# Kernel optimization log

Hardware: AMD Instinct MI355X
Metric: run time of the kernel (lower is better)

The kernel has to match this reference:

```python
import jax, jax.numpy as jnp
import numpy as np

N, E = 50000, 640000
DIN, DH, DOUT = 128, 256, 128


def _glorot(k, i, o):
    return jax.random.normal(k, (i, o), jnp.float32) / np.sqrt(i)


def setup_inputs() -> dict:
    key = jax.random.key(0)
    ks = jax.random.split(key, 12)
    return {
        "x": jax.random.normal(ks[0], (N, DIN), jnp.float32),
        "edge_index": jax.random.randint(ks[1], (2, E), 0, N, dtype=jnp.int32),
        # SAGEConv 1: in -> hidden (lin_l on aggregated w/ bias, lin_r on root)
        "W1l": _glorot(ks[2], DIN, DH), "b1l": jnp.zeros((DH,), jnp.float32), "W1r": _glorot(ks[3], DIN, DH),
        "g1": jnp.ones((DH,), jnp.float32), "be1": jnp.zeros((DH,), jnp.float32),
        # skip projection (in != hidden)
        "Wsk": _glorot(ks[4], DIN, DH), "bsk": jnp.zeros((DH,), jnp.float32),
        # SAGEConv 2: hidden -> hidden
        "W2l": _glorot(ks[5], DH, DH), "b2l": jnp.zeros((DH,), jnp.float32), "W2r": _glorot(ks[6], DH, DH),
        "g2": jnp.ones((DH,), jnp.float32), "be2": jnp.zeros((DH,), jnp.float32),
        # SAGEConv 3: hidden -> out
        "W3l": _glorot(ks[7], DH, DOUT), "b3l": jnp.zeros((DOUT,), jnp.float32), "W3r": _glorot(ks[8], DH, DOUT),
    }


def _sage_conv(x, src, dst, Wl, bl, Wr, n):
    # mean aggregation of source features into destination nodes
    msg = x[src]                                                 # [E, d]
    agg = jax.ops.segment_sum(msg, dst, num_segments=n)          # [N, d]
    cnt = jax.ops.segment_sum(jnp.ones((src.shape[0],), x.dtype), dst, num_segments=n)
    agg = agg / jnp.maximum(cnt, 1.0)[:, None]
    return agg @ Wl + bl + x @ Wr


def _layernorm(x, g, b):
    mu = jnp.mean(x, axis=-1, keepdims=True)
    var = jnp.mean((x - mu) ** 2, axis=-1, keepdims=True)
    return (x - mu) * jax.lax.rsqrt(var + 1e-5) * g + b


def reference(x, edge_index, W1l, b1l, W1r, g1, be1, Wsk, bsk,
              W2l, b2l, W2r, g2, be2, W3l, b3l, W3r):
    src, dst = edge_index[0], edge_index[1]
    n = x.shape[0]
    # layer 0: conv -> LN -> relu -> (dropout p=0, eval) -> skip via projection
    h = _sage_conv(x, src, dst, W1l, b1l, W1r, n)
    h = jax.nn.relu(_layernorm(h, g1, be1))
    h = h + (x @ Wsk + bsk)
    # layer 1: conv -> LN -> relu -> residual add (shapes match)
    h2 = _sage_conv(h, src, dst, W2l, b2l, W2r, n)
    h2 = jax.nn.relu(_layernorm(h2, g2, be2)) + h
    # final conv (no norm/act)
    return _sage_conv(h2, src, dst, W3l, b3l, W3r, n)
```

## Files before the change

### kernel.cpp

```cpp
#include <hip/hip_runtime.h>


typedef float floatx4 __attribute__((ext_vector_type(4)));
typedef float floatx2 __attribute__((ext_vector_type(2)));
typedef short bf16x8 __attribute__((ext_vector_type(8)));

__device__ inline unsigned short f2bf(float f) {
    unsigned u = __float_as_uint(f);
    unsigned r = (u + 0x7fffu + ((u >> 16) & 1u)) >> 16;
    return (unsigned short)r;
}
__device__ inline float bf2f_lo(unsigned v) { return __uint_as_float(v << 16); }
__device__ inline float bf2f_hi(unsigned v) { return __uint_as_float(v & 0xffff0000u); }

__device__ inline void gl_lds16(const void* g, void* l) {
    __builtin_amdgcn_global_load_lds((const __attribute__((address_space(1))) unsigned int*)g,
                                     (__attribute__((address_space(3))) unsigned int*)l,
                                     16, 0, 0);
}

__global__ void hist_kernel(const int* __restrict__ dst, int* __restrict__ cnt, int E) {
    int i = blockIdx.x * blockDim.x + threadIdx.x;
    if (i < E) atomicAdd(&cnt[dst[i]], 1);
}

#define SCAN_CHUNK 2048

__global__ __launch_bounds__(256) void scan_blocksums(const int* __restrict__ cnt,
                                                      int* __restrict__ bsum, int N) {
    __shared__ int sh[256];
    int t = threadIdx.x;
    int base = blockIdx.x * SCAN_CHUNK + t * 8;
    int s = 0;
#pragma unroll
    for (int i = 0; i < 8; i++) {
        int idx = base + i;
        if (idx < N) s += cnt[idx];
    }
    sh[t] = s;
    __syncthreads();
    for (int off = 1; off < 256; off <<= 1) {
        int v = (t >= off) ? sh[t - off] : 0;
        __syncthreads();
        sh[t] += v;
        __syncthreads();
    }
    if (t == 255) bsum[blockIdx.x] = sh[255];
}

__global__ __launch_bounds__(256) void scan_bsums(const int* __restrict__ bsum,
                                                  int* __restrict__ boff, int NB,
                                                  int* __restrict__ rowptr, int N, int E) {
    __shared__ int sh[256];
    int t = threadIdx.x;
    int v = (t < NB) ? bsum[t] : 0;
    sh[t] = v;
    __syncthreads();
    for (int off = 1; off < 256; off <<= 1) {
        int u = (t >= off) ? sh[t - off] : 0;
        __syncthreads();
        sh[t] += u;
        __syncthreads();
    }
    if (t < NB) boff[t] = sh[t] - v;
    if (t == 0) rowptr[N] = E;
}

__global__ __launch_bounds__(256) void scan_final(const int* __restrict__ cnt,
                                                  const int* __restrict__ boff,
                                                  int* __restrict__ rowptr,
                                                  int* __restrict__ cursor,
                                                  float* __restrict__ invdeg, int N) {
    __shared__ int sh[256];
    int t = threadIdx.x;
    int base = blockIdx.x * SCAN_CHUNK + t * 8;
    int c[8];
    int s = 0;
#pragma unroll
    for (int i = 0; i < 8; i++) {
        int idx = base + i;
        c[i] = (idx < N) ? cnt[idx] : 0;
        s += c[i];
    }
    sh[t] = s;
    __syncthreads();
    for (int off = 1; off < 256; off <<= 1) {
        int v = (t >= off) ? sh[t - off] : 0;
        __syncthreads();
        sh[t] += v;
        __syncthreads();
    }
    int run = boff[blockIdx.x] + sh[t] - s;
#pragma unroll
    for (int i = 0; i < 8; i++) {
        int idx = base + i;
        if (idx < N) {
            rowptr[idx] = run;
            cursor[idx] = run;
            invdeg[idx] = 1.0f / (float)(c[i] > 1 ? c[i] : 1);
            run += c[i];
        }
    }
}

__global__ void scatter_kernel(const int* __restrict__ src, const int* __restrict__ dst,
                               int* __restrict__ cursor, int* __restrict__ col, int E) {
    int i = blockIdx.x * blockDim.x + threadIdx.x;
    if (i < E) {
        int p = atomicAdd(&cursor[dst[i]], 1);
        col[p] = src[i];
    }
}

__global__ void prep_weights(const float* __restrict__ W1l, const float* __restrict__ W1r,
                             const float* __restrict__ Wsk, const float* __restrict__ W2l,
                             const float* __restrict__ W2r, const float* __restrict__ W3l,
                             const float* __restrict__ W3r, const float* __restrict__ b1l,
                             const float* __restrict__ bsk,
                             unsigned short* __restrict__ WtC, unsigned short* __restrict__ Wt2,
                             unsigned short* __restrict__ Wt3, float* __restrict__ biasC) {
    int i = blockIdx.x * blockDim.x + threadIdx.x;
    if (i < 32768) {
        int k = i >> 8, n = i & 255;
        WtC[n * 256 + k] = f2bf(W1l[i]);
    } else if (i < 65536) {
        int j = i - 32768, k = j >> 8, n = j & 255;
        WtC[n * 256 + 128 + k] = f2bf(W1r[j]);
    } else if (i < 98304) {
        int j = i - 65536, k = j >> 8, n = j & 255;
        WtC[(256 + n) * 256 + 128 + k] = f2bf(Wsk[j]);
    } else if (i < 131072) {
        int j = i - 98304, k = j >> 8, n = j & 255;
        WtC[(256 + n) * 256 + k] = 0;
    } else if (i < 196608) {
        int j = i - 131072, k = j >> 8, n = j & 255;
        Wt2[n * 512 + k] = f2bf(W2l[j]);
    } else if (i < 262144) {
        int j = i - 196608, k = j >> 8, n = j & 255;
        Wt2[n * 512 + 256 + k] = f2bf(W2r[j]);
    } else if (i < 294912) {
        int j = i - 262144, k = j >> 7, n = j & 127;
        Wt3[n * 256 + k] = f2bf(W3l[j]);
    } else if (i < 327680) {
        int j = i - 294912, k = j >> 7, n = j & 127;
        Wt3[(128 + n) * 256 + k] = f2bf(W3r[j]);
    } else if (i < 328192) {
        int j = i - 327680;
        biasC[j] = (j < 256) ? b1l[j] : bsk[j - 256];
    }
}

__global__ void cvt_x2(const float* __restrict__ x, unsigned short* __restrict__ A1cat,
                       unsigned char* __restrict__ X8, int total32) {
    int i = blockIdx.x * blockDim.x + threadIdx.x;
    if (i >= total32) return;
    int r = i >> 5, c4 = (i & 31) * 4;
    float4 v = *(const float4*)(x + (size_t)r * 128 + c4);
    ushort4 o;
    o.x = f2bf(v.x); o.y = f2bf(v.y); o.z = f2bf(v.z); o.w = f2bf(v.w);
    *(ushort4*)(A1cat + (size_t)r * 256 + 128 + c4) = o;
    unsigned wpk = 0;
    wpk = __builtin_amdgcn_cvt_pk_fp8_f32(v.x, v.y, wpk, false);
    wpk = __builtin_amdgcn_cvt_pk_fp8_f32(v.z, v.w, wpk, true);
    *(unsigned*)(X8 + (size_t)r * 128 + c4) = wpk;
}

__device__ inline void accum_fp8(uint2 v, float m, float* a) {
    floatx2 p;
    p = __builtin_amdgcn_cvt_pk_f32_fp8(v.x, false); a[0] = fmaf(m, p.x, a[0]); a[1] = fmaf(m, p.y, a[1]);
    p = __builtin_amdgcn_cvt_pk_f32_fp8(v.x, true);  a[2] = fmaf(m, p.x, a[2]); a[3] = fmaf(m, p.y, a[3]);
    p = __builtin_amdgcn_cvt_pk_f32_fp8(v.y, false); a[4] = fmaf(m, p.x, a[4]); a[5] = fmaf(m, p.y, a[5]);
    p = __builtin_amdgcn_cvt_pk_f32_fp8(v.y, true);  a[6] = fmaf(m, p.x, a[6]); a[7] = fmaf(m, p.y, a[7]);
}

template <int RSB>
__global__ __launch_bounds__(256) void agg_fp8_c(const int* __restrict__ rowptr,
                                                 const int* __restrict__ col,
                                                 const float* __restrict__ invdeg,
                                                 const unsigned char* __restrict__ T8,
                                                 unsigned short* __restrict__ out, int ostride, int N) {
    int wid = (blockIdx.x * blockDim.x + threadIdx.x) >> 6;
    int lane = threadIdx.x & 63;
    if (wid >= N) return;
    int co = blockIdx.y * 64;
    int sub = lane & 7;
    int g = lane >> 3;
    const unsigned char* To = T8 + co + sub * 8;
    int s = rowptr[wid], e = rowptr[wid + 1];
    float a[8] = {0.f, 0.f, 0.f, 0.f, 0.f, 0.f, 0.f, 0.f};
    for (int j = s + g; j < e; j += 32) {
        int j1 = (j + 8 < e) ? j + 8 : j;
        int j2 = (j + 16 < e) ? j + 16 : j;
        int j3 = (j + 24 < e) ? j + 24 : j;
        float m1 = (j + 8 < e) ? 1.f : 0.f;
        float m2 = (j + 16 < e) ? 1.f : 0.f;
        float m3 = (j + 24 < e) ? 1.f : 0.f;
        int c0 = col[j], c1 = col[j1], c2 = col[j2], c3 = col[j3];
        uint2 v0 = *(const uint2*)(To + (size_t)c0 * RSB);
        uint2 v1 = *(const uint2*)(To + (size_t)c1 * RSB);
        uint2 v2 = *(const uint2*)(To + (size_t)c2 * RSB);
        uint2 v3 = *(const uint2*)(To + (size_t)c3 * RSB);
        accum_fp8(v0, 1.f, a);
        accum_fp8(v1, m1, a);
        accum_fp8(v2, m2, a);
        accum_fp8(v3, m3, a);
    }
#pragma unroll
    for (int i = 0; i < 8; i++) {
        a[i] += __shfl_xor(a[i], 8, 64);
        a[i] += __shfl_xor(a[i], 16, 64);
        a[i] += __shfl_xor(a[i], 32, 64);
    }
    if (g == 0) {
        float inv = invdeg[wid];
        uint4 o;
        o.x = (unsigned)f2bf(a[0] * inv) | ((unsigned)f2bf(a[1] * inv) << 16);
        o.y = (unsigned)f2bf(a[2] * inv) | ((unsigned)f2bf(a[3] * inv) << 16);
        o.z = (unsigned)f2bf(a[4] * inv) | ((unsigned)f2bf(a[5] * inv) << 16);
        o.w = (unsigned)f2bf(a[6] * inv) | ((unsigned)f2bf(a[7] * inv) << 16);
        *(uint4*)(out + (size_t)wid * ostride + co + sub * 8) = o;
    }
}

__global__ __launch_bounds__(256) void agg_fin_c(const int* __restrict__ rowptr,
                                                 const int* __restrict__ col,
                                                 const float* __restrict__ invdeg,
                                                 const unsigned short* __restrict__ T,
                                                 const float* __restrict__ R,
                                                 float* __restrict__ out, int N) {
    int wid = (blockIdx.x * blockDim.x + threadIdx.x) >> 6;
    int lane = threadIdx.x & 63;
    if (wid >= N) return;
    int co2 = blockIdx.y * 32;
    int sub = lane & 7;
    int g = lane >> 3;
    const unsigned short* To = T + co2 + sub * 4;
    int s = rowptr[wid], e = rowptr[wid + 1];
    float a0 = 0.f, a1 = 0.f, a2 = 0.f, a3 = 0.f;
    for (int j = s + g; j < e; j += 32) {
        int j1 = (j + 8 < e) ? j + 8 : j;
        int j2 = (j + 16 < e) ? j + 16 : j;
        int j3 = (j + 24 < e) ? j + 24 : j;
        float m1 = (j + 8 < e) ? 1.f : 0.f;
        float m2 = (j + 16 < e) ? 1.f : 0.f;
        float m3 = (j + 24 < e) ? 1.f : 0.f;
        int c0 = col[j], c1 = col[j1], c2 = col[j2], c3 = col[j3];
        uint2 v0 = *(const uint2*)(To + (size_t)c0 * 128);
        uint2 v1 = *(const uint2*)(To + (size_t)c1 * 128);
        uint2 v2 = *(const uint2*)(To + (size_t)c2 * 128);
        uint2 v3 = *(const uint2*)(To + (size_t)c3 * 128);
        a0 += bf2f_lo(v0.x); a1 += bf2f_hi(v0.x); a2 += bf2f_lo(v0.y); a3 += bf2f_hi(v0.y);
        a0 = fmaf(m1, bf2f_lo(v1.x), a0); a1 = fmaf(m1, bf2f_hi(v1.x), a1);
        a2 = fmaf(m1, bf2f_lo(v1.y), a2); a3 = fmaf(m1, bf2f_hi(v1.y), a3);
        a0 = fmaf(m2, bf2f_lo(v2.x), a0); a1 = fmaf(m2, bf2f_hi(v2.x), a1);
        a2 = fmaf(m2, bf2f_lo(v2.y), a2); a3 = fmaf(m2, bf2f_hi(v2.y), a3);
        a0 = fmaf(m3, bf2f_lo(v3.x), a0); a1 = fmaf(m3, bf2f_hi(v3.x), a1);
        a2 = fmaf(m3, bf2f_lo(v3.y), a2); a3 = fmaf(m3, bf2f_hi(v3.y), a3);
    }
#pragma unroll
    for (int off = 8; off < 64; off <<= 1) {
        a0 += __shfl_xor(a0, off, 64);
        a1 += __shfl_xor(a1, off, 64);
        a2 += __shfl_xor(a2, off, 64);
        a3 += __shfl_xor(a3, off, 64);
    }
    if (g == 0) {
        float inv = invdeg[wid];
        float4 r = *(const float4*)(R + (size_t)wid * 128 + co2 + sub * 4);
        float4 o;
        o.x = a0 * inv + r.x;
        o.y = a1 * inv + r.y;
        o.z = a2 * inv + r.z;
        o.w = a3 * inv + r.w;
        *(float4*)(out + (size_t)wid * 128 + co2 + sub * 4) = o;
    }
}

template <int KIT, int NPAN, int MODE>
__global__ __launch_bounds__(512) void gemm_fused(
    const unsigned short* __restrict__ A, int lda,
    const unsigned short* __restrict__ B, int ldb,
    const float* __restrict__ bias,
    const float* __restrict__ gamma, const float* __restrict__ beta,
    const unsigned short* __restrict__ resid,
    unsigned short* __restrict__ outb,
    unsigned char* __restrict__ h8,
    float* __restrict__ outf, int M) {
    constexpr int COLS = NPAN * 256;
    constexpr int LNW = COLS + 8;
    constexpr int STAGE_E = 128 * 64;
    constexpr int STAGE_F = 2 * STAGE_E / 2;
    constexpr int SMEM_F = (STAGE_F > 32 * LNW) ? STAGE_F : 32 * LNW;
    __shared__ __align__(16) float smemf[SMEM_F];
    unsigned short* sbase = (unsigned short*)smemf;

    int t = threadIdx.x;
    int lane = t & 63, w = t >> 6;
    int bm = blockIdx.x * 128;
    int wm = (w & 1) * 64, wn = (w >> 1) * 64;
    int m16 = lane & 15, kq = lane >> 4;

    floatx4 acc[NPAN][4][4];
#pragma unroll
    for (int p = 0; p < NPAN; p++)
#pragma unroll
        for (int i = 0; i < 4; i++)
#pragma unroll
            for (int j = 0; j < 4; j++) acc[p][i][j] = (floatx4){0.f, 0.f, 0.f, 0.f};

    const int s_row0 = t >> 3;
    const int s_j = t & 7;

    auto stage = [&](int kt, int bsel) {
        unsigned short* s = sbase + bsel * STAGE_E;
        int k0 = kt * 64;
#pragma unroll
        for (int i = 0; i < 2; i++) {
            int row = s_row0 + i * 64;
            int kc = s_j ^ (row & 7);
            int rowA = bm + row;
            if (rowA > M - 1) rowA = M - 1;
            gl_lds16(A + (size_t)rowA * lda + k0 + kc * 8, (void*)&s[(size_t)(i * 512 + t) * 8]);
        }
    };

    stage(0, 0);
    __syncthreads();
    for (int kt = 0; kt < KIT; kt++) {
        if (kt + 1 < KIT) stage(kt + 1, (kt & 1) ^ 1);
        const unsigned short* sA = sbase + (kt & 1) * STAGE_E;
#pragma unroll
        for (int ks = 0; ks < 2; ks++) {
            int kcl = (ks << 2) | kq;
            bf16x8 af[4];
#pragma unroll
            for (int mi = 0; mi < 4; mi++)
                af[mi] = *(const bf16x8*)&sA[(wm + mi * 16 + m16) * 64 + (kcl ^ (m16 & 7)) * 8];
#pragma unroll
            for (int p = 0; p < NPAN; p++) {
                if (MODE == 0 && p == 1 && kt * 64 < 128) continue;
                const unsigned short* Bp = B + (size_t)(wn + p * 256) * ldb + kt * 64;
                bf16x8 bf[4];
#pragma unroll
                for (int ni = 0; ni < 4; ni++)
                    bf[ni] = *(const bf16x8*)&Bp[(size_t)(ni * 16 + m16) * ldb + kcl * 8];
#pragma unroll
                for (int mi = 0; mi < 4; mi++)
#pragma unroll
                    for (int ni = 0; ni < 4; ni++)
                        acc[p][mi][ni] =
                            __builtin_amdgcn_mfma_f32_16x16x32_bf16(af[mi], bf[ni], acc[p][mi][ni], 0, 0, 0);
            }
        }
        __syncthreads();
    }

    float* lnb = smemf;
    int c4 = lane * 4;
    float4 bu = {0.f, 0.f, 0.f, 0.f}, bs = {0.f, 0.f, 0.f, 0.f};
    float4 gv = {0.f, 0.f, 0.f, 0.f}, bv = {0.f, 0.f, 0.f, 0.f};
    float4 b3 = {0.f, 0.f, 0.f, 0.f};
    if (MODE == 0) {
        bu = *(const float4*)&bias[c4];
        bs = *(const float4*)&bias[256 + c4];
        gv = *(const float4*)&gamma[c4];
        bv = *(const float4*)&beta[c4];
    } else if (MODE == 1) {
        bu = *(const float4*)&bias[c4];
        gv = *(const float4*)&gamma[c4];
        bv = *(const float4*)&beta[c4];
    } else {
        if (lane >= 32) b3 = *(const float4*)&bias[c4 - 128];
    }

#pragma unroll
    for (int g4 = 0; g4 < 4; g4++) {
        if (wm == (g4 >> 1) * 64) {
            int mi0 = (g4 & 1) * 2;
#pragma unroll
            for (int p = 0; p < NPAN; p++)
#pragma unroll
                for (int mm = 0; mm < 2; mm++)
#pragma unroll
                    for (int ni = 0; ni < 4; ni++)
#pragma unroll
                        for (int r = 0; r < 4; r++)
                            lnb[(mm * 16 + kq * 4 + r) * LNW + wn + p * 256 + ni * 16 + m16] =
                                acc[p][mi0 + mm][ni][r];
        }
        __syncthreads();
#pragma unroll
        for (int rr = 0; rr < 4; rr++) {
            int lrow = w * 4 + rr;
            int grow = bm + g4 * 32 + lrow;
            bool valid = grow < M;
            float4 u = *(const float4*)&lnb[lrow * LNW + c4];
            if (MODE <= 1) {
                u.x += bu.x; u.y += bu.y; u.z += bu.z; u.w += bu.w;
                float s1 = (u.x + u.y) + (u.z + u.w);
                float s2 = (u.x * u.x + u.y * u.y) + (u.z * u.z + u.w * u.w);
#pragma unroll
                for (int off = 1; off < 64; off <<= 1) {
                    s1 += __shfl_xor(s1, off, 64);
                    s2 += __shfl_xor(s2, off, 64);
                }
                float mu = s1 * (1.f / 256.f);
                float var = s2 * (1.f / 256.f) - mu * mu;
                float rs = rsqrtf(var + 1e-5f);
                float a0, a1, a2, a3;
                if (MODE == 0) {
                    float4 sv = *(const float4*)&lnb[lrow * LNW + 256 + c4];
                    a0 = sv.x + bs.x; a1 = sv.y + bs.y; a2 = sv.z + bs.z; a3 = sv.w + bs.w;
                } else {
                    int gr = valid ? grow : M - 1;
                    uint2 hv = *(const uint2*)(resid + (size_t)gr * 512 + c4);
                    a0 = bf2f_lo(hv.x); a1 = bf2f_hi(hv.x); a2 = bf2f_lo(hv.y); a3 = bf2f_hi(hv.y);
                }
                float o0 = fmaxf((u.x - mu) * rs * gv.x + bv.x, 0.f) + a0;
                float o1 = fmaxf((u.y - mu) * rs * gv.y + bv.y, 0.f) + a1;
                float o2 = fmaxf((u.z - mu) * rs * gv.z + bv.z, 0.f) + a2;
                float o3 = fmaxf((u.w - mu) * rs * gv.w + bv.w, 0.f) + a3;
                if (valid) {
                    ushort4 o;
                    o.x = f2bf(o0); o.y = f2bf(o1); o.z = f2bf(o2); o.w = f2bf(o3);
                    *(ushort4*)(outb + (size_t)grow * 512 + c4) = o;
                    if (MODE == 0) {
                        unsigned wpk = 0;
                        wpk = __builtin_amdgcn_cvt_pk_fp8_f32(o0, o1, wpk, false);
                        wpk = __builtin_amdgcn_cvt_pk_fp8_f32(o2, o3, wpk, true);
                        *(unsigned*)(h8 + (size_t)grow * 256 + c4) = wpk;
                    }
                }
            } else {
                if (valid) {
                    if (lane < 32) {
                        ushort4 o;
                        o.x = f2bf(u.x); o.y = f2bf(u.y); o.z = f2bf(u.z); o.w = f2bf(u.w);
                        *(ushort4*)(outb + (size_t)grow * 128 + c4) = o;
                    } else {
                        float4 o;
                        o.x = u.x + b3.x; o.y = u.y + b3.y; o.z = u.z + b3.z; o.w = u.w + b3.w;
                        *(float4*)(outf + (size_t)grow * 128 + (c4 - 128)) = o;
                    }
                }
            }
        }
        __syncthreads();
    }
}

extern "C" void kernel_launch(void* const* d_in, const int* in_sizes, int n_in,
                              void* d_out, int out_size, void* d_ws, size_t ws_size,
                              hipStream_t stream) {
    const float* x   = (const float*)d_in[0];
    const int*   ei  = (const int*)d_in[1];
    const float* W1l = (const float*)d_in[2];
    const float* b1l = (const float*)d_in[3];
    const float* W1r = (const float*)d_in[4];
    const float* g1  = (const float*)d_in[5];
    const float* be1 = (const float*)d_in[6];
    const float* Wsk = (const float*)d_in[7];
    const float* bsk = (const float*)d_in[8];
    const float* W2l = (const float*)d_in[9];
    const float* b2l = (const float*)d_in[10];
    const float* W2r = (const float*)d_in[11];
    const float* g2  = (const float*)d_in[12];
    const float* be2 = (const float*)d_in[13];
    const float* W3l = (const float*)d_in[14];
    const float* b3l = (const float*)d_in[15];
    const float* W3r = (const float*)d_in[16];

    const int N = in_sizes[0] / 128;
    const int E = in_sizes[1] / 2;
    const int* src = ei;
    const int* dst = ei + E;

    char* p = (char*)d_ws;
    auto alloc = [&](size_t bytes) {
        void* r = (void*)p;
        p += (bytes + 255) & ~(size_t)255;
        return r;
    };
    int*   cnt    = (int*)alloc(sizeof(int) * N);
    int*   rowptr = (int*)alloc(sizeof(int) * (N + 1));
    int*   cursor = (int*)alloc(sizeof(int) * N);
    float* invdeg = (float*)alloc(sizeof(float) * N);
    int*   col    = (int*)alloc(sizeof(int) * E);
    int*   bsum   = (int*)alloc(sizeof(int) * 256);
    int*   boff   = (int*)alloc(sizeof(int) * 256);
    unsigned short* A1cat = (unsigned short*)alloc(sizeof(short) * (size_t)N * 256);
    unsigned short* A2cat = (unsigned short*)alloc(sizeof(short) * (size_t)N * 512);
    float* r3 = (float*)alloc(sizeof(float) * (size_t)N * 128);
    unsigned char* H8 = (unsigned char*)alloc((size_t)N * 256);
    unsigned char* X8 = (unsigned char*)alloc((size_t)N * 128);
    unsigned short* WtC = (unsigned short*)alloc(sizeof(short) * 512 * 256);
    unsigned short* Wt2 = (unsigned short*)alloc(sizeof(short) * 256 * 512);
    unsigned short* Wt3 = (unsigned short*)alloc(sizeof(short) * 256 * 256);
    float* biasC = (float*)alloc(sizeof(float) * 512);
    unsigned short* t3 = A1cat;

    hipMemsetAsync(cnt, 0, sizeof(int) * N, stream);
    hist_kernel<<<(E + 255) / 256, 256, 0, stream>>>(dst, cnt, E);
    int NB = (N + SCAN_CHUNK - 1) / SCAN_CHUNK;
    scan_blocksums<<<NB, 256, 0, stream>>>(cnt, bsum, N);
    scan_bsums<<<1, 256, 0, stream>>>(bsum, boff, NB, rowptr, N, E);
    scan_final<<<NB, 256, 0, stream>>>(cnt, boff, rowptr, cursor, invdeg, N);
    scatter_kernel<<<(E + 255) / 256, 256, 0, stream>>>(src, dst, cursor, col, E);

    prep_weights<<<(328192 + 255) / 256, 256, 0, stream>>>(W1l, W1r, Wsk, W2l, W2r, W3l, W3r,
                                                           b1l, bsk, WtC, Wt2, Wt3, biasC);
    cvt_x2<<<((N * 32) + 255) / 256, 256, 0, stream>>>(x, A1cat, X8, N * 32);

    int aggBlocks = (N + 3) / 4;
    int mBlocks = (N + 127) / 128;

    agg_fp8_c<128><<<dim3(aggBlocks, 2), 256, 0, stream>>>(rowptr, col, invdeg, X8, A1cat, 256, N);
    gemm_fused<4, 2, 0><<<mBlocks, 512, 0, stream>>>(A1cat, 256, WtC, 256, biasC, g1, be1,
                                                     nullptr, A2cat + 256, H8, nullptr, N);

    agg_fp8_c<256><<<dim3(aggBlocks, 4), 256, 0, stream>>>(rowptr, col, invdeg, H8, A2cat, 512, N);
    gemm_fused<8, 1, 1><<<mBlocks, 512, 0, stream>>>(A2cat, 512, Wt2, 512, b2l, g2, be2,
                                                     A2cat + 256, A2cat, nullptr, nullptr, N);

    gemm_fused<4, 1, 2><<<mBlocks, 512, 0, stream>>>(A2cat, 512, Wt3, 256, b3l, nullptr, nullptr,
                                                     nullptr, t3, nullptr, r3, N);
    agg_fin_c<<<dim3(aggBlocks, 4), 256, 0, stream>>>(rowptr, col, invdeg, t3, r3, (float*)d_out, N);
}
```

Measured before the change: 469.9 us.

## Map lane groups to whole nodes in aggregation kernels with wider loads

The aggregation kernels no longer give each node a full wavefront split over column chunks in a 2D grid with a cross-lane shuffle reduction. Each group of lanes now covers one node's full feature row, so a wavefront handles several nodes. Each lane does 16-byte gathers and accumulates with packed float2 math. This removes the shuffle reduction, the redundant rowptr/col reads repeated per column block, and the idle lanes on low-degree nodes. In exchange, each node's neighbours are walked serially by its lane group, so high-degree nodes can cause load imbalance within a wavefront.

New measurement: 376.9 us. 19.8% less time.

```diff
diff --git a/kernel.cpp b/kernel.cpp
--- a/kernel.cpp
+++ b/kernel.cpp
@@ -165,64 +165,75 @@
     *(unsigned*)(X8 + (size_t)r * 128 + c4) = wpk;
 }
 
-__device__ inline void accum_fp8(uint2 v, float m, float* a) {
+__device__ inline void acc16_fp8(uint4 v, float m, floatx2* a) {
+    floatx2 mm = {m, m};
     floatx2 p;
-    p = __builtin_amdgcn_cvt_pk_f32_fp8(v.x, false); a[0] = fmaf(m, p.x, a[0]); a[1] = fmaf(m, p.y, a[1]);
-    p = __builtin_amdgcn_cvt_pk_f32_fp8(v.x, true);  a[2] = fmaf(m, p.x, a[2]); a[3] = fmaf(m, p.y, a[3]);
-    p = __builtin_amdgcn_cvt_pk_f32_fp8(v.y, false); a[4] = fmaf(m, p.x, a[4]); a[5] = fmaf(m, p.y, a[5]);
-    p = __builtin_amdgcn_cvt_pk_f32_fp8(v.y, true);  a[6] = fmaf(m, p.x, a[6]); a[7] = fmaf(m, p.y, a[7]);
+    p = __builtin_amdgcn_cvt_pk_f32_fp8(v.x, false); a[0] = p * mm + a[0];
+    p = __builtin_amdgcn_cvt_pk_f32_fp8(v.x, true);  a[1] = p * mm + a[1];
+    p = __builtin_amdgcn_cvt_pk_f32_fp8(v.y, false); a[2] = p * mm + a[2];
+    p = __builtin_amdgcn_cvt_pk_f32_fp8(v.y, true);  a[3] = p * mm + a[3];
+    p = __builtin_amdgcn_cvt_pk_f32_fp8(v.z, false); a[4] = p * mm + a[4];
+    p = __builtin_amdgcn_cvt_pk_f32_fp8(v.z, true);  a[5] = p * mm + a[5];
+    p = __builtin_amdgcn_cvt_pk_f32_fp8(v.w, false); a[6] = p * mm + a[6];
+    p = __builtin_amdgcn_cvt_pk_f32_fp8(v.w, true);  a[7] = p * mm + a[7];
 }
 
 template <int RSB>
-__global__ __launch_bounds__(256) void agg_fp8_c(const int* __restrict__ rowptr,
+__global__ __launch_bounds__(256) void agg_fp8_g(const int* __restrict__ rowptr,
                                                  const int* __restrict__ col,
                                                  const float* __restrict__ invdeg,
                                                  const unsigned char* __restrict__ T8,
                                                  unsigned short* __restrict__ out, int ostride, int N) {
+    constexpr int LPR = RSB / 16;
+    constexpr int NPW = 64 / LPR;
     int wid = (blockIdx.x * blockDim.x + threadIdx.x) >> 6;
     int lane = threadIdx.x & 63;
-    if (wid >= N) return;
-    int co = blockIdx.y * 64;
-    int sub = lane & 7;
-    int g = lane >> 3;
-    const unsigned char* To = T8 + co + sub * 8;
-    int s = rowptr[wid], e = rowptr[wid + 1];
-    float a[8] = {0.f, 0.f, 0.f, 0.f, 0.f, 0.f, 0.f, 0.f};
-    for (int j = s + g; j < e; j += 32) {
-        int j1 = (j + 8 < e) ? j + 8 : j;
-        int j2 = (j + 16 < e) ? j + 16 : j;
-        int j3 = (j + 24 < e) ? j + 24 : j;
-        float m1 = (j + 8 < e) ? 1.f : 0.f;
-        float m2 = (j + 16 < e) ? 1.f : 0.f;
-        float m3 = (j + 24 < e) ? 1.f : 0.f;
+    int sub = lane & (LPR - 1);
+    int g = lane / LPR;
+    int node = wid * NPW + g;
+    bool vn = node < N;
+    int nc = vn ? node : N - 1;
+    int s = rowptr[nc];
+    int e = vn ? rowptr[nc + 1] : s;
+    const unsigned char* To = T8 + sub * 16;
+    floatx2 a[8];
+#pragma unroll
+    for (int i = 0; i < 8; i++) a[i] = (floatx2){0.f, 0.f};
+    for (int j = s; j < e; j += 4) {
+        int j1 = (j + 1 < e) ? j + 1 : j;
+        int j2 = (j + 2 < e) ? j + 2 : j;
+        int j3 = (j + 3 < e) ? j + 3 : j;
+        float m1 = (j + 1 < e) ? 1.f : 0.f;
+        float m2 = (j + 2 < e) ? 1.f : 0.f;
+        float m3 = (j + 3 < e) ? 1.f : 0.f;
         int c0 = col[j], c1 = col[j1], c2 = col[j2], c3 = col[j3];
-        uint2 v0 = *(const uint2*)(To + (size_t)c0 * RSB);
-        uint2 v1 = *(const uint2*)(To + (size_t)c1 * RSB);
-        uint2 v2 = *(const uint2*)(To + (size_t)c2 * RSB);
-        uint2 v3 = *(const uint2*)(To + (size_t)c3 * RSB);
-        accum_fp8(v0, 1.f, a);
-        accum_fp8(v1, m1, a);
-        accum_fp8(v2, m2, a);
-        accum_fp8(v3, m3, a);
-    }
-#pragma unroll
-    for (int i = 0; i < 8; i++) {
-        a[i] += __shfl_xor(a[i], 8, 64);
-        a[i] += __shfl_xor(a[i], 16, 64);
-        a[i] += __shfl_xor(a[i], 32, 64);
-    }
-    if (g == 0) {
-        float inv = invdeg[wid];
-        uint4 o;
-        o.x = (unsigned)f2bf(a[0] * inv) | ((unsigned)f2bf(a[1] * inv) << 16);
-        o.y = (unsigned)f2bf(a[2] * inv) | ((unsigned)f2bf(a[3] * inv) << 16);
-        o.z = (unsigned)f2bf(a[4] * inv) | ((unsigned)f2bf(a[5] * inv) << 16);
-        o.w = (unsigned)f2bf(a[6] * inv) | ((unsigned)f2bf(a[7] * inv) << 16);
-        *(uint4*)(out + (size_t)wid * ostride + co + sub * 8) = o;
-    }
-}
-
-__global__ __launch_bounds__(256) void agg_fin_c(const int* __restrict__ rowptr,
+        uint4 v0 = *(const uint4*)(To + (size_t)c0 * RSB);
+        uint4 v1 = *(const uint4*)(To + (size_t)c1 * RSB);
+        uint4 v2 = *(const uint4*)(To + (size_t)c2 * RSB);
+        uint4 v3 = *(const uint4*)(To + (size_t)c3 * RSB);
+        acc16_fp8(v0, 1.f, a);
+        acc16_fp8(v1, m1, a);
+        acc16_fp8(v2, m2, a);
+        acc16_fp8(v3, m3, a);
+    }
+    if (vn) {
+        float inv = invdeg[node];
+        uint4 o1, o2;
+        o1.x = (unsigned)f2bf(a[0].x * inv) | ((unsigned)f2bf(a[0].y * inv) << 16);
+        o1.y = (unsigned)f2bf(a[1].x * inv) | ((unsigned)f2bf(a[1].y * inv) << 16);
+        o1.z = (unsigned)f2bf(a[2].x * inv) | ((unsigned)f2bf(a[2].y * inv) << 16);
+        o1.w = (unsigned)f2bf(a[3].x * inv) | ((unsigned)f2bf(a[3].y * inv) << 16);
+        o2.x = (unsigned)f2bf(a[4].x * inv) | ((unsigned)f2bf(a[4].y * inv) << 16);
+        o2.y = (unsigned)f2bf(a[5].x * inv) | ((unsigned)f2bf(a[5].y * inv) << 16);
+        o2.z = (unsigned)f2bf(a[6].x * inv) | ((unsigned)f2bf(a[6].y * inv) << 16);
+        o2.w = (unsigned)f2bf(a[7].x * inv) | ((unsigned)f2bf(a[7].y * inv) << 16);
+        unsigned short* op = out + (size_t)node * ostride + sub * 16;
+        *(uint4*)op = o1;
+        *(uint4*)(op + 8) = o2;
+    }
+}
+
+__global__ __launch_bounds__(256) void agg_fin_g(const int* __restrict__ rowptr,
                                                  const int* __restrict__ col,
                                                  const float* __restrict__ invdeg,
                                                  const unsigned short* __restrict__ T,
@@ -230,49 +241,65 @@
                                                  float* __restrict__ out, int N) {
     int wid = (blockIdx.x * blockDim.x + threadIdx.x) >> 6;
     int lane = threadIdx.x & 63;
-    if (wid >= N) return;
-    int co2 = blockIdx.y * 32;
-    int sub = lane & 7;
-    int g = lane >> 3;
-    const unsigned short* To = T + co2 + sub * 4;
-    int s = rowptr[wid], e = rowptr[wid + 1];
-    float a0 = 0.f, a1 = 0.f, a2 = 0.f, a3 = 0.f;
-    for (int j = s + g; j < e; j += 32) {
-        int j1 = (j + 8 < e) ? j + 8 : j;
-        int j2 = (j + 16 < e) ? j + 16 : j;
-        int j3 = (j + 24 < e) ? j + 24 : j;
-        float m1 = (j + 8 < e) ? 1.f : 0.f;
-        float m2 = (j + 16 < e) ? 1.f : 0.f;
-        float m3 = (j + 24 < e) ? 1.f : 0.f;
+    int sub = lane & 15;
+    int g = lane >> 4;
+    int node = wid * 4 + g;
+    bool vn = node < N;
+    int nc = vn ? node : N - 1;
+    int s = rowptr[nc];
+    int e = vn ? rowptr[nc + 1] : s;
+    const unsigned short* To = T + sub * 8;
+    floatx2 a[4];
+#pragma unroll
+    for (int i = 0; i < 4; i++) a[i] = (floatx2){0.f, 0.f};
+    for (int j = s; j < e; j += 4) {
+        int j1 = (j + 1 < e) ? j + 1 : j;
+        int j2 = (j + 2 < e) ? j + 2 : j;
+        int j3 = (j + 3 < e) ? j + 3 : j;
+        float m1 = (j + 1 < e) ? 1.f : 0.f;
+        float m2 = (j + 2 < e) ? 1.f : 0.f;
+        float m3 = (j + 3 < e) ? 1.f : 0.f;
         int c0 = col[j], c1 = col[j1], c2 = col[j2], c3 = col[j3];
-        uint2 v0 = *(const uint2*)(To + (size_t)c0 * 128);
-        uint2 v1 = *(const uint2*)(To + (size_t)c1 * 128);
-        uint2 v2 = *(const uint2*)(To + (size_t)c2 * 128);
-        uint2 v3 = *(const uint2*)(To + (size_t)c3 * 128);
-        a0 += bf2f_lo(v0.x); a1 += bf2f_hi(v0.x); a2 += bf2f_lo(v0.y); a3 += bf2f_hi(v0.y);
-        a0 = fmaf(m1, bf2f_lo(v1.x), a0); a1 = fmaf(m1, bf2f_hi(v1.x), a1);
-        a2 = fmaf(m1, bf2f_lo(v1.y), a2); a3 = fmaf(m1, bf2f_hi(v1.y), a3);
-        a0 = fmaf(m2, bf2f_lo(v2.x), a0); a1 = fmaf(m2, bf2f_hi(v2.x), a1);
-        a2 = fmaf(m2, bf2f_lo(v2.y), a2); a3 = fmaf(m2, bf2f_hi(v2.y), a3);
-        a0 = fmaf(m3, bf2f_lo(v3.x), a0); a1 = fmaf(m3, bf2f_hi(v3.x), a1);
-        a2 = fmaf(m3, bf2f_lo(v3.y), a2); a3 = fmaf(m3, bf2f_hi(v3.y), a3);
-    }
-#pragma unroll
-    for (int off = 8; off < 64; off <<= 1) {
-        a0 += __shfl_xor(a0, off, 64);
-        a1 += __shfl_xor(a1, off, 64);
-        a2 += __shfl_xor(a2, off, 64);
-        a3 += __shfl_xor(a3, off, 64);
-    }
-    if (g == 0) {
-        float inv = invdeg[wid];
-        float4 r = *(const float4*)(R + (size_t)wid * 128 + co2 + sub * 4);
-        float4 o;
-        o.x = a0 * inv + r.x;
-        o.y = a1 * inv + r.y;
-        o.z = a2 * inv + r.z;
-        o.w = a3 * inv + r.w;
-        *(float4*)(out + (size_t)wid * 128 + co2 + sub * 4) = o;
+        uint4 v0 = *(const uint4*)(To + (size_t)c0 * 128);
+        uint4 v1 = *(const uint4*)(To + (size_t)c1 * 128);
+        uint4 v2 = *(const uint4*)(To + (size_t)c2 * 128);
+        uint4 v3 = *(const uint4*)(To + (size_t)c3 * 128);
+        floatx2 mm;
+        floatx2 p;
+        mm = (floatx2){1.f, 1.f};
+        p = (floatx2){bf2f_lo(v0.x), bf2f_hi(v0.x)}; a[0] = p + a[0];
+        p = (floatx2){bf2f_lo(v0.y), bf2f_hi(v0.y)}; a[1] = p + a[1];
+        p = (floatx2){bf2f_lo(v0.z), bf2f_hi(v0.z)}; a[2] = p + a[2];
+        p = (floatx2){bf2f_lo(v0.w), bf2f_hi(v0.w)}; a[3] = p + a[3];
+        mm = (floatx2){m1, m1};
+        p = (floatx2){bf2f_lo(v1.x), bf2f_hi(v1.x)}; a[0] = p * mm + a[0];
+        p = (floatx2){bf2f_lo(v1.y), bf2f_hi(v1.y)}; a[1] = p * mm + a[1];
+        p = (floatx2){bf2f_lo(v1.z), bf2f_hi(v1.z)}; a[2] = p * mm + a[2];
+        p = (floatx2){bf2f_lo(v1.w), bf2f_hi(v1.w)}; a[3] = p * mm + a[3];
+        mm = (floatx2){m2, m2};
+        p = (floatx2){bf2f_lo(v2.x), bf2f_hi(v2.x)}; a[0] = p * mm + a[0];
+        p = (floatx2){bf2f_lo(v2.y), bf2f_hi(v2.y)}; a[1] = p * mm + a[1];
+        p = (floatx2){bf2f_lo(v2.z), bf2f_hi(v2.z)}; a[2] = p * mm + a[2];
+        p = (floatx2){bf2f_lo(v2.w), bf2f_hi(v2.w)}; a[3] = p * mm + a[3];
+        mm = (floatx2){m3, m3};
+        p = (floatx2){bf2f_lo(v3.x), bf2f_hi(v3.x)}; a[0] = p * mm + a[0];
+        p = (floatx2){bf2f_lo(v3.y), bf2f_hi(v3.y)}; a[1] = p * mm + a[1];
+        p = (floatx2){bf2f_lo(v3.z), bf2f_hi(v3.z)}; a[2] = p * mm + a[2];
+        p = (floatx2){bf2f_lo(v3.w), bf2f_hi(v3.w)}; a[3] = p * mm + a[3];
+    }
+    if (vn) {
+        float inv = invdeg[node];
+        const float* Rp = R + (size_t)node * 128 + sub * 8;
+        float4 r1 = *(const float4*)Rp;
+        float4 r2 = *(const float4*)(Rp + 4);
+        float4 o1, o2;
+        o1.x = a[0].x * inv + r1.x; o1.y = a[0].y * inv + r1.y;
+        o1.z = a[1].x * inv + r1.z; o1.w = a[1].y * inv + r1.w;
+        o2.x = a[2].x * inv + r2.x; o2.y = a[2].y * inv + r2.y;
+        o2.z = a[3].x * inv + r2.z; o2.w = a[3].y * inv + r2.w;
+        float* op = out + (size_t)node * 128 + sub * 8;
+        *(float4*)op = o1;
+        *(float4*)(op + 4) = o2;
     }
 }
 
@@ -511,18 +538,20 @@
                                                            b1l, bsk, WtC, Wt2, Wt3, biasC);
     cvt_x2<<<((N * 32) + 255) / 256, 256, 0, stream>>>(x, A1cat, X8, N * 32);
 
-    int aggBlocks = (N + 3) / 4;
     int mBlocks = (N + 127) / 128;
-
-    agg_fp8_c<128><<<dim3(aggBlocks, 2), 256, 0, stream>>>(rowptr, col, invdeg, X8, A1cat, 256, N);
+    int agg1Blocks = (N + 31) / 32;
+    int agg2Blocks = (N + 15) / 16;
+    int aggFBlocks = (N + 15) / 16;
+
+    agg_fp8_g<128><<<agg1Blocks, 256, 0, stream>>>(rowptr, col, invdeg, X8, A1cat, 256, N);
     gemm_fused<4, 2, 0><<<mBlocks, 512, 0, stream>>>(A1cat, 256, WtC, 256, biasC, g1, be1,
                                                      nullptr, A2cat + 256, H8, nullptr, N);
 
-    agg_fp8_c<256><<<dim3(aggBlocks, 4), 256, 0, stream>>>(rowptr, col, invdeg, H8, A2cat, 512, N);
+    agg_fp8_g<256><<<agg2Blocks, 256, 0, stream>>>(rowptr, col, invdeg, H8, A2cat, 512, N);
     gemm_fused<8, 1, 1><<<mBlocks, 512, 0, stream>>>(A2cat, 512, Wt2, 512, b2l, g2, be2,
                                                      A2cat + 256, A2cat, nullptr, nullptr, N);
 
     gemm_fused<4, 1, 2><<<mBlocks, 512, 0, stream>>>(A2cat, 512, Wt3, 256, b3l, nullptr, nullptr,
                                                      nullptr, t3, nullptr, r3, N);
-    agg_fin_c<<<dim3(aggBlocks, 4), 256, 0, stream>>>(rowptr, col, invdeg, t3, r3, (float*)d_out, N);
-}
+    agg_fin_g<<<aggFBlocks, 256, 0, stream>>>(rowptr, col, invdeg, t3, r3, (float*)d_out, N);
+}
```
